# Optimization experiments

Hardware: AMD Instinct MI355X
Metric: run time of the kernel (lower is better)

Reference implementation:

```python
import jax, jax.numpy as jnp
import numpy as np

B, S, D = 4, 2048, 1024
H = 16
HD = D // H          # 64
HALF = HD // 2       # 32


def _rope(t, cos, sin):
    # t: [B, S, H, HD]; cos/sin: [S, HALF]
    tr = t.reshape(*t.shape[:-1], HALF, 2)
    t0, t1 = tr[..., 0], tr[..., 1]
    c = cos[None, :, None, :]
    s = sin[None, :, None, :]
    out = jnp.stack([t0 * c - t1 * s, t0 * s + t1 * c], axis=-1)
    return out.reshape(t.shape)


def setup_inputs() -> dict:
    key = jax.random.key(0)
    ks = jax.random.split(key, 7)
    x = jax.random.normal(ks[0], (B, S, D), dtype=jnp.float32)
    # rotary tables (theta=10000 convention)
    inv_freq = 1.0 / (10000.0 ** (np.arange(0, HD, 2, dtype=np.float32) / HD))
    angles = np.arange(S, dtype=np.float32)[:, None] * inv_freq[None, :]
    freqs_cos = jnp.asarray(np.cos(angles))
    freqs_sin = jnp.asarray(np.sin(angles))
    scale = 1.0 / np.sqrt(D)
    wq = jax.random.normal(ks[1], (D, D), dtype=jnp.float32) * scale
    wk = jax.random.normal(ks[2], (D, D), dtype=jnp.float32) * scale
    wv = jax.random.normal(ks[3], (D, D), dtype=jnp.float32) * scale
    wo = jax.random.normal(ks[4], (D, D), dtype=jnp.float32) * scale
    return {"x": x, "freqs_cos": freqs_cos, "freqs_sin": freqs_sin,
            "wq": wq, "wk": wk, "wv": wv, "wo": wo}


def reference(x, freqs_cos, freqs_sin, wq, wk, wv, wo):
    b, s, d = x.shape
    q = (x @ wq.T).reshape(b, s, H, HD)
    k = (x @ wk.T).reshape(b, s, H, HD)
    v = (x @ wv.T).reshape(b, s, H, HD)
    q = _rope(q, freqs_cos, freqs_sin)
    k = _rope(k, freqs_cos, freqs_sin)
    # [B, H, S, HD]
    q = q.transpose(0, 2, 1, 3)
    k = k.transpose(0, 2, 1, 3)
    v = v.transpose(0, 2, 1, 3)
    scores = jnp.einsum("bhqd,bhkd->bhqk", q, k) / jnp.sqrt(jnp.float32(HD))
    causal = jnp.tril(jnp.ones((s, s), dtype=bool))
    scores = jnp.where(causal[None, None, :, :], scores, jnp.finfo(scores.dtype).min)
    attn = jax.nn.softmax(scores, axis=-1)
    out = jnp.einsum("bhqk,bhkd->bhqd", attn, v)
    out = out.transpose(0, 2, 1, 3).reshape(b, s, d)
    return out @ wo.T
```

## Files before the change

### kernel.cpp

```cpp
#include <hip/hip_runtime.h>
#include <hip/hip_bf16.h>
#include <cstdint>
#include <cstddef>

#define BB 4
#define SS 2048
#define DD 1024
#define HH 16
#define HDD 64

typedef __bf16 bf16_t;
typedef __bf16 bf16x8 __attribute__((ext_vector_type(8)));
typedef float f32x4 __attribute__((ext_vector_type(4)));
typedef unsigned u32x2 __attribute__((ext_vector_type(2)));

__device__ __forceinline__ unsigned short f2bf(float f) {
    unsigned u = __float_as_uint(f);
    unsigned r = (u + 0x7FFFu + ((u >> 16) & 1u)) >> 16;
    return (unsigned short)r;
}
__device__ __forceinline__ bf16_t f2bf16(float f) {
    return __builtin_bit_cast(bf16_t, f2bf(f));
}
__device__ __forceinline__ bf16x8 cvt8(float4 a, float4 b) {
    bf16x8 r;
    r[0] = f2bf16(a.x); r[1] = f2bf16(a.y);
    r[2] = f2bf16(a.z); r[3] = f2bf16(a.w);
    r[4] = f2bf16(b.x); r[5] = f2bf16(b.y);
    r[6] = f2bf16(b.z); r[7] = f2bf16(b.w);
    return r;
}
__device__ __forceinline__ unsigned cvtpk_bf16(float lo, float hi) {
    unsigned r;
    asm("v_cvt_pk_bf16_f32 %0, %1, %2" : "=v"(r) : "v"(lo), "v"(hi));
    return r;
}
__device__ __forceinline__ float exp2_raw(float x) {
    float r;
    asm("v_exp_f32 %0, %1" : "=v"(r) : "v"(x));
    return r;
}

#define GLL16(gp, lp)                                                          \
    __builtin_amdgcn_global_load_lds(                                          \
        (const __attribute__((address_space(1))) void*)(gp),                   \
        (__attribute__((address_space(3))) void*)(lp), 16, 0, 0)

__global__ __launch_bounds__(256) void cvtall(
    const float* __restrict__ x,
    const float* __restrict__ w0, const float* __restrict__ w1,
    const float* __restrict__ w2, const float* __restrict__ w3,
    bf16_t* __restrict__ xb,
    bf16_t* __restrict__ o0, bf16_t* __restrict__ o1,
    bf16_t* __restrict__ o2, bf16_t* __restrict__ o3)
{
    const int bx = blockIdx.x;
    const float* in;
    bf16_t* out;
    size_t i;
    if (bx < 4096) {
        in = x; out = xb;
        i = (size_t)bx * 256 + threadIdx.x;
    } else {
        const int g = bx - 4096;
        const int s = g >> 9;
        in  = s == 0 ? w0 : s == 1 ? w1 : s == 2 ? w2 : w3;
        out = s == 0 ? o0 : s == 1 ? o1 : s == 2 ? o2 : o3;
        i = (size_t)(g & 511) * 256 + threadIdx.x;
    }
    const float4* p = (const float4*)in + i * 2;
    *(bf16x8*)(out + i * 8) = cvt8(p[0], p[1]);
}

__global__ __launch_bounds__(256, 2) void gemm_qkv(
    const bf16_t* __restrict__ A, const bf16_t* __restrict__ Wall,
    bf16_t* __restrict__ Qb, bf16_t* __restrict__ Kb,
    bf16_t* __restrict__ Vt,
    const float* __restrict__ fcos, const float* __restrict__ fsin,
    float qscale)
{
    constexpr int K = 1024;
    __shared__ alignas(16) bf16_t lA[128 * 64];
    __shared__ alignas(16) bf16_t lB[128 * 64];

    const int tid  = threadIdx.x;
    const int w    = tid >> 6;
    const int lane = tid & 63;
    const int quad = lane >> 4;
    const int l16  = lane & 15;
    const int wm   = w >> 1;
    const int wn   = w & 1;

    const int lid     = blockIdx.y * 24 + blockIdx.x;
    const int logical = (lid & 7) * 192 + (lid >> 3);
    const int m0      = (logical / 24) * 128;
    const int n0      = (logical % 24) * 128;
    const int sub     = n0 >> 10;

    f32x4 acc[4][4];
#pragma unroll
    for (int i = 0; i < 4; i++)
#pragma unroll
        for (int j = 0; j < 4; j++) acc[i][j] = (f32x4){0.f, 0.f, 0.f, 0.f};

    const int srow8 = lane >> 3;
    const int slot  = lane & 7;

    for (int k0 = 0; k0 < K; k0 += 64) {
#pragma unroll
        for (int i = 0; i < 4; ++i) {
            int rbase = w * 32 + i * 8;
            int row   = rbase + srow8;
            int sc    = (slot ^ (row & 7)) * 8;
            GLL16(A + (size_t)(m0 + row) * K + k0 + sc, &lA[rbase * 64]);
            GLL16(Wall + (size_t)(n0 + row) * K + k0 + sc, &lB[rbase * 64]);
        }
        __syncthreads();
#pragma unroll
        for (int kk = 0; kk < 2; ++kk) {
            bf16x8 af[4], bfr[4];
#pragma unroll
            for (int mt = 0; mt < 4; ++mt) {
                const int row = wm * 64 + mt * 16 + l16;
                af[mt] = *(const bf16x8*)
                    &lA[row * 64 + (((kk * 4 + quad) ^ (row & 7)) * 8)];
            }
#pragma unroll
            for (int nt = 0; nt < 4; ++nt) {
                const int row = wn * 64 + nt * 16 + l16;
                bfr[nt] = *(const bf16x8*)
                    &lB[row * 64 + (((kk * 4 + quad) ^ (row & 7)) * 8)];
            }
#pragma unroll
            for (int mt = 0; mt < 4; ++mt)
#pragma unroll
                for (int nt = 0; nt < 4; ++nt)
                    acc[mt][nt] = __builtin_amdgcn_mfma_f32_16x16x32_bf16(
                        af[mt], bfr[nt], acc[mt][nt], 0, 0, 0);
        }
        __syncthreads();
    }

    if (sub < 2) {
        unsigned short* Cu = (unsigned short*)(sub == 0 ? Qb : Kb);
        const float scale = sub == 0 ? qscale : 1.0f;
#pragma unroll
        for (int mt = 0; mt < 4; ++mt) {
#pragma unroll
            for (int nt = 0; nt < 4; ++nt) {
                int col  = (n0 & 1023) + wn * 64 + nt * 16 + l16;
                int h    = col >> 6;
                int d    = col & 63;
                int pidx = d >> 1;
                bool even = (col & 1) == 0;
#pragma unroll
                for (int r = 0; r < 4; ++r) {
                    int m = m0 + wm * 64 + mt * 16 + quad * 4 + r;
                    int b = m >> 11;
                    int s = m & 2047;
                    float v  = acc[mt][nt][r];
                    float p  = __shfl_xor(v, 1);
                    float c  = fcos[s * 32 + pidx];
                    float sn = fsin[s * 32 + pidx];
                    float o  = even ? (v * c - p * sn) : (p * sn + v * c);
                    Cu[(size_t)((b * HH + h) * SS + s) * HDD + d] =
                        f2bf(o * scale);
                }
            }
        }
    } else {
        unsigned short* Cu = (unsigned short*)Vt;
#pragma unroll
        for (int mt = 0; mt < 4; ++mt) {
#pragma unroll
            for (int nt = 0; nt < 4; ++nt) {
                int col = (n0 & 1023) + wn * 64 + nt * 16 + l16;
                int h = col >> 6, d = col & 63;
#pragma unroll
                for (int r = 0; r < 4; ++r) {
                    int m = m0 + wm * 64 + mt * 16 + quad * 4 + r;
                    int b = m >> 11, s = m & 2047;
                    Cu[(size_t)((b * HH + h) * HDD + d) * SS + s] =
                        f2bf(acc[mt][nt][r]);
                }
            }
        }
    }
}

__global__ __launch_bounds__(256, 2) void gemm_out(
    const bf16_t* __restrict__ A, const bf16_t* __restrict__ W,
    float* __restrict__ Cf)
{
    constexpr int K = 1024, N = 1024;
    __shared__ alignas(16) bf16_t lA[128 * 64];
    __shared__ alignas(16) bf16_t lB[128 * 64];

    const int tid  = threadIdx.x;
    const int w    = tid >> 6;
    const int lane = tid & 63;
    const int quad = lane >> 4;
    const int l16  = lane & 15;
    const int wm   = w >> 1;
    const int wn   = w & 1;

    const int lid     = blockIdx.y * 8 + blockIdx.x;
    const int logical = (lid & 7) * 64 + (lid >> 3);
    const int m0      = (logical >> 3) * 128;
    const int n0      = (logical & 7) * 128;

    f32x4 acc[4][4];
#pragma unroll
    for (int i = 0; i < 4; i++)
#pragma unroll
        for (int j = 0; j < 4; j++) acc[i][j] = (f32x4){0.f, 0.f, 0.f, 0.f};

    const int srow8 = lane >> 3;
    const int slot  = lane & 7;

    for (int k0 = 0; k0 < K; k0 += 64) {
#pragma unroll
        for (int i = 0; i < 4; ++i) {
            int rbase = w * 32 + i * 8;
            int row   = rbase + srow8;
            int sc    = (slot ^ (row & 7)) * 8;
            GLL16(A + (size_t)(m0 + row) * K + k0 + sc, &lA[rbase * 64]);
            GLL16(W + (size_t)(n0 + row) * K + k0 + sc, &lB[rbase * 64]);
        }
        __syncthreads();
#pragma unroll
        for (int kk = 0; kk < 2; ++kk) {
            bf16x8 af[4], bfr[4];
#pragma unroll
            for (int mt = 0; mt < 4; ++mt) {
                const int row = wm * 64 + mt * 16 + l16;
                af[mt] = *(const bf16x8*)
                    &lA[row * 64 + (((kk * 4 + quad) ^ (row & 7)) * 8)];
            }
#pragma unroll
            for (int nt = 0; nt < 4; ++nt) {
                const int row = wn * 64 + nt * 16 + l16;
                bfr[nt] = *(const bf16x8*)
                    &lB[row * 64 + (((kk * 4 + quad) ^ (row & 7)) * 8)];
            }
#pragma unroll
            for (int mt = 0; mt < 4; ++mt)
#pragma unroll
                for (int nt = 0; nt < 4; ++nt)
                    acc[mt][nt] = __builtin_amdgcn_mfma_f32_16x16x32_bf16(
                        af[mt], bfr[nt], acc[mt][nt], 0, 0, 0);
        }
        __syncthreads();
    }

#pragma unroll
    for (int mt = 0; mt < 4; ++mt) {
        int mrow = m0 + wm * 64 + mt * 16 + quad * 4;
#pragma unroll
        for (int nt = 0; nt < 4; ++nt) {
            int col = n0 + wn * 64 + nt * 16 + l16;
#pragma unroll
            for (int r = 0; r < 4; ++r)
                Cf[(size_t)(mrow + r) * N + col] = acc[mt][nt][r];
        }
    }
}

__global__ __launch_bounds__(256, 2) void attn(
    const bf16_t* __restrict__ Q, const bf16_t* __restrict__ Kt,
    const bf16_t* __restrict__ Vt, bf16_t* __restrict__ O)
{
    __shared__ alignas(16) bf16_t lK[128 * 64];
    __shared__ alignas(16) bf16_t lV[2][64 * 64];

    const int tid  = threadIdx.x;
    const int w    = tid >> 6;
    const int lane = tid & 63;
    const int quad = lane >> 4;
    const int l16  = lane & 15;

    const int blk  = blockIdx.x;
    const int xcd  = blk & 7;
    const int rest = blk >> 3;
    const int g    = rest & 7;
    const int bh   = ((rest >> 3) << 3) | xcd;

    const int b = bh >> 4, h = bh & 15;
    unsigned short* Ou = (unsigned short*)O;
    const bf16_t* Qb = Q  + (size_t)bh * SS * HDD;
    const bf16_t* Kb = Kt + (size_t)bh * SS * HDD;
    const bf16_t* Vb = Vt + (size_t)bh * HDD * SS;

    const int row8 = lane >> 3;
    const int chk  = lane & 7;

    for (int phase = 0; phase < 2; ++phase) {
        const int Tp  = phase ? 15 - g : g;
        const int q0  = Tp * 128 + w * 32;
        const int nkb = Tp + 1;

        bf16x8 qf[2][2];
#pragma unroll
        for (int qs = 0; qs < 2; ++qs) {
            const bf16_t* qp =
                Qb + (size_t)(q0 + qs * 16 + l16) * HDD + quad * 8;
            qf[qs][0] = *(const bf16x8*)(qp);
            qf[qs][1] = *(const bf16x8*)(qp + 32);
        }

        f32x4 o[2][4];
        float ps[2];
#pragma unroll
        for (int qs = 0; qs < 2; ++qs) {
            ps[qs] = 0.f;
#pragma unroll
            for (int i = 0; i < 4; ++i) o[qs][i] = (f32x4){0.f, 0.f, 0.f, 0.f};
        }

        for (int t = 0; t < nkb; ++t) {
            const int kb2 = t * 128;

#pragma unroll
            for (int i = 0; i < 4; ++i) {
                int rbase = w * 32 + i * 8;
                int row   = rbase + row8;
                GLL16(Kb + (size_t)(kb2 + row) * HDD + ((chk ^ (row & 7)) * 8),
                      &lK[rbase * 64]);
            }
#pragma unroll
            for (int pp = 0; pp < 2; ++pp)
#pragma unroll
                for (int i = 0; i < 2; ++i) {
                    int rbase = w * 16 + i * 8;
                    int row   = rbase + row8;
                    GLL16(Vb + (size_t)row * SS + kb2 + pp * 64 +
                              ((chk ^ (row & 7)) * 8),
                          &lV[pp][rbase * 64]);
                }
            __syncthreads();

#pragma unroll
            for (int p = 0; p < 2; ++p) {
                const int kbp = kb2 + p * 64;
                if (kbp < q0 + 32) {
                    const bool diag = (kbp + 63 > q0);

                    bf16x8 kf[4][2];
#pragma unroll
                    for (int nt = 0; nt < 4; ++nt) {
                        const int row = p * 64 + nt * 16 + l16;
#pragma unroll
                        for (int hf = 0; hf < 2; ++hf)
                            kf[nt][hf] = *(const bf16x8*)
                                &lK[row * 64 +
                                    (((hf * 4 + quad) ^ (row & 7)) * 8)];
                    }

                    unsigned pk[4][2][2];
#pragma unroll
                    for (int nt = 0; nt < 4; ++nt) {
                        const int krow = kbp + nt * 16 + quad * 4;
#pragma unroll
                        for (int qs = 0; qs < 2; ++qs) {
                            f32x4 s = (f32x4){0.f, 0.f, 0.f, 0.f};
                            s = __builtin_amdgcn_mfma_f32_16x16x32_bf16(
                                kf[nt][0], qf[qs][0], s, 0, 0, 0);
                            s = __builtin_amdgcn_mfma_f32_16x16x32_bf16(
                                kf[nt][1], qf[qs][1], s, 0, 0, 0);
                            if (diag) {
                                const int qcol = q0 + qs * 16 + l16;
#pragma unroll
                                for (int r = 0; r < 4; ++r)
                                    if (krow + r > qcol) s[r] = -1e30f;
                            }
                            float ev[4];
#pragma unroll
                            for (int r = 0; r < 4; ++r) {
                                float e = exp2_raw(s[r]);
                                ps[qs] += e;
                                ev[r] = e;
                            }
                            pk[nt][qs][0] = cvtpk_bf16(ev[0], ev[1]);
                            pk[nt][qs][1] = cvtpk_bf16(ev[2], ev[3]);
                        }
                    }

#pragma unroll
                    for (int kk = 0; kk < 2; ++kk) {
                        bf16x8 vfk[4];
#pragma unroll
                        for (int nt = 0; nt < 4; ++nt) {
                            const int row = nt * 16 + l16;
                            vfk[nt] = *(const bf16x8*)
                                &lV[p][row * 64 +
                                       (((kk * 4 + quad) ^ (row & 7)) * 8)];
                        }
#pragma unroll
                        for (int qs = 0; qs < 2; ++qs) {
                            u32x2 sA = __builtin_amdgcn_permlane32_swap(
                                pk[2 * kk][qs][0], pk[2 * kk + 1][qs][0],
                                false, false);
                            u32x2 sB = __builtin_amdgcn_permlane32_swap(
                                pk[2 * kk][qs][1], pk[2 * kk + 1][qs][1],
                                false, false);
                            u32x2 tA = __builtin_amdgcn_permlane16_swap(
                                sA.x, sA.y, false, false);
                            u32x2 tB = __builtin_amdgcn_permlane16_swap(
                                sB.x, sB.y, false, false);
                            union { unsigned d[4]; bf16x8 v; } pf;
                            pf.d[0] = tA.x;
                            pf.d[1] = tB.x;
                            pf.d[2] = tA.y;
                            pf.d[3] = tB.y;
#pragma unroll
                            for (int nt = 0; nt < 4; ++nt)
                                o[qs][nt] =
                                    __builtin_amdgcn_mfma_f32_16x16x32_bf16(
                                        pf.v, vfk[nt], o[qs][nt], 0, 0, 0);
                        }
                    }
                }
            }
            __syncthreads();
        }

#pragma unroll
        for (int qs = 0; qs < 2; ++qs) {
            float tsum = ps[qs];
            tsum += __shfl_xor(tsum, 16);
            tsum += __shfl_xor(tsum, 32);
            float inv[4];
#pragma unroll
            for (int r = 0; r < 4; ++r)
                inv[r] = 1.0f / __shfl(tsum, quad * 4 + r);
#pragma unroll
            for (int nt = 0; nt < 4; ++nt) {
                int d = nt * 16 + l16;
#pragma unroll
                for (int r = 0; r < 4; ++r) {
                    int s = q0 + qs * 16 + quad * 4 + r;
                    Ou[(size_t)(b * SS + s) * DD + h * HDD + d] =
                        f2bf(o[qs][nt][r] * inv[r]);
                }
            }
        }
    }
}

extern "C" void kernel_launch(void* const* d_in, const int* in_sizes, int n_in,
                              void* d_out, int out_size, void* d_ws,
                              size_t ws_size, hipStream_t stream)
{
    const float* x    = (const float*)d_in[0];
    const float* fcos = (const float*)d_in[1];
    const float* fsin = (const float*)d_in[2];
    const float* wq   = (const float*)d_in[3];
    const float* wk   = (const float*)d_in[4];
    const float* wv   = (const float*)d_in[5];
    const float* wo   = (const float*)d_in[6];

    char* ws = (char*)d_ws;
    const size_t TSZ = (size_t)BB * SS * DD * sizeof(bf16_t);
    const size_t WSZ = (size_t)DD * DD * sizeof(bf16_t);
    bf16_t* Qb  = (bf16_t*)(ws);
    bf16_t* Kb  = (bf16_t*)(ws + TSZ);
    bf16_t* Ob  = (bf16_t*)(ws + 2 * TSZ);
    bf16_t* wb0 = (bf16_t*)(ws + 3 * TSZ);
    bf16_t* wb1 = (bf16_t*)(ws + 3 * TSZ + WSZ);
    bf16_t* wb2 = (bf16_t*)(ws + 3 * TSZ + 2 * WSZ);
    bf16_t* wb3 = (bf16_t*)(ws + 3 * TSZ + 3 * WSZ);
    bf16_t* xb  = (bf16_t*)d_out;
    bf16_t* Vt  = (bf16_t*)((char*)d_out + TSZ);

    dim3 bb(256);
    cvtall<<<dim3(6144), bb, 0, stream>>>(x, wq, wk, wv, wo,
                                          xb, wb0, wb1, wb2, wb3);

    const float sscale = 0.125f * 1.44269504088896f;
    gemm_qkv<<<dim3(24, 64), bb, 0, stream>>>(xb, wb0, Qb, Kb, Vt,
                                              fcos, fsin, sscale);
    attn<<<dim3(512), bb, 0, stream>>>(Qb, Kb, Vt, Ob);
    gemm_out<<<dim3(8, 64), bb, 0, stream>>>(Ob, wb3, (float*)d_out);
}
```

Baseline: 229.6 us.

## Merge QKV and output GEMMs into templated 256x128 tile kernel with 8 waves

Replaces the two separate 128x128 GEMM kernels with one templated kernel using 512 threads and a 256-row M tile, sharing the B tile across twice as many rows. This is meant to cut global and LDS traffic per MFMA and halve the block count. The epilogue is selected by a template MODE: RoPE/scatter for QKV, or a plain fp32 store for the output projection. Larger LDS use and the doubled block size may reduce occupancy, and fewer blocks may underfill the GPU.

```diff
diff --git a/kernel.cpp b/kernel.cpp
--- a/kernel.cpp
+++ b/kernel.cpp
@@ -72,15 +72,16 @@
     *(bf16x8*)(out + i * 8) = cvt8(p[0], p[1]);
 }
 
-__global__ __launch_bounds__(256, 2) void gemm_qkv(
-    const bf16_t* __restrict__ A, const bf16_t* __restrict__ Wall,
+template <int MODE, int NT>
+__global__ __launch_bounds__(512, 2) void gemm256(
+    const bf16_t* __restrict__ A, const bf16_t* __restrict__ W,
     bf16_t* __restrict__ Qb, bf16_t* __restrict__ Kb,
-    bf16_t* __restrict__ Vt,
+    bf16_t* __restrict__ Vt, float* __restrict__ Cf,
     const float* __restrict__ fcos, const float* __restrict__ fsin,
     float qscale)
 {
     constexpr int K = 1024;
-    __shared__ alignas(16) bf16_t lA[128 * 64];
+    __shared__ alignas(16) bf16_t lA[256 * 64];
     __shared__ alignas(16) bf16_t lB[128 * 64];
 
     const int tid  = threadIdx.x;
@@ -91,11 +92,11 @@
     const int wm   = w >> 1;
     const int wn   = w & 1;
 
-    const int lid     = blockIdx.y * 24 + blockIdx.x;
-    const int logical = (lid & 7) * 192 + (lid >> 3);
-    const int m0      = (logical / 24) * 128;
-    const int n0      = (logical % 24) * 128;
-    const int sub     = n0 >> 10;
+    const int lid     = blockIdx.y * NT + blockIdx.x;
+    constexpr int CHK = (NT * 32) >> 3;
+    const int logical = (lid & 7) * CHK + (lid >> 3);
+    const int m0      = (logical / NT) * 256;
+    const int n0      = (logical % NT) * 128;
 
     f32x4 acc[4][4];
 #pragma unroll
@@ -103,17 +104,23 @@
 #pragma unroll
         for (int j = 0; j < 4; j++) acc[i][j] = (f32x4){0.f, 0.f, 0.f, 0.f};
 
-    const int srow8 = lane >> 3;
-    const int slot  = lane & 7;
+    const int row8 = lane >> 3;
+    const int chk  = lane & 7;
 
     for (int k0 = 0; k0 < K; k0 += 64) {
 #pragma unroll
         for (int i = 0; i < 4; ++i) {
             int rbase = w * 32 + i * 8;
-            int row   = rbase + srow8;
-            int sc    = (slot ^ (row & 7)) * 8;
-            GLL16(A + (size_t)(m0 + row) * K + k0 + sc, &lA[rbase * 64]);
-            GLL16(Wall + (size_t)(n0 + row) * K + k0 + sc, &lB[rbase * 64]);
+            int row   = rbase + row8;
+            GLL16(A + (size_t)(m0 + row) * K + k0 + ((chk ^ (row & 7)) * 8),
+                  &lA[rbase * 64]);
+        }
+#pragma unroll
+        for (int i = 0; i < 2; ++i) {
+            int rbase = w * 16 + i * 8;
+            int row   = rbase + row8;
+            GLL16(W + (size_t)(n0 + row) * K + k0 + ((chk ^ (row & 7)) * 8),
+                  &lB[rbase * 64]);
         }
         __syncthreads();
 #pragma unroll
@@ -141,127 +148,64 @@
         __syncthreads();
     }
 
-    if (sub < 2) {
-        unsigned short* Cu = (unsigned short*)(sub == 0 ? Qb : Kb);
-        const float scale = sub == 0 ? qscale : 1.0f;
+    if (MODE == 0) {
+        const int sub = n0 >> 10;
+        if (sub < 2) {
+            unsigned short* Cu = (unsigned short*)(sub == 0 ? Qb : Kb);
+            const float scale = sub == 0 ? qscale : 1.0f;
+#pragma unroll
+            for (int mt = 0; mt < 4; ++mt) {
+#pragma unroll
+                for (int nt = 0; nt < 4; ++nt) {
+                    int col  = (n0 & 1023) + wn * 64 + nt * 16 + l16;
+                    int h    = col >> 6;
+                    int d    = col & 63;
+                    int pidx = d >> 1;
+                    bool even = (col & 1) == 0;
+#pragma unroll
+                    for (int r = 0; r < 4; ++r) {
+                        int m = m0 + wm * 64 + mt * 16 + quad * 4 + r;
+                        int b = m >> 11;
+                        int s = m & 2047;
+                        float v  = acc[mt][nt][r];
+                        float p  = __shfl_xor(v, 1);
+                        float c  = fcos[s * 32 + pidx];
+                        float sn = fsin[s * 32 + pidx];
+                        float o  = even ? (v * c - p * sn) : (p * sn + v * c);
+                        Cu[(size_t)((b * HH + h) * SS + s) * HDD + d] =
+                            f2bf(o * scale);
+                    }
+                }
+            }
+        } else {
+            unsigned short* Cu = (unsigned short*)Vt;
+#pragma unroll
+            for (int mt = 0; mt < 4; ++mt) {
+#pragma unroll
+                for (int nt = 0; nt < 4; ++nt) {
+                    int col = (n0 & 1023) + wn * 64 + nt * 16 + l16;
+                    int h = col >> 6, d = col & 63;
+#pragma unroll
+                    for (int r = 0; r < 4; ++r) {
+                        int m = m0 + wm * 64 + mt * 16 + quad * 4 + r;
+                        int b = m >> 11, s = m & 2047;
+                        Cu[(size_t)((b * HH + h) * HDD + d) * SS + s] =
+                            f2bf(acc[mt][nt][r]);
+                    }
+                }
+            }
+        }
+    } else {
 #pragma unroll
         for (int mt = 0; mt < 4; ++mt) {
+            int mrow = m0 + wm * 64 + mt * 16 + quad * 4;
 #pragma unroll
             for (int nt = 0; nt < 4; ++nt) {
-                int col  = (n0 & 1023) + wn * 64 + nt * 16 + l16;
-                int h    = col >> 6;
-                int d    = col & 63;
-                int pidx = d >> 1;
-                bool even = (col & 1) == 0;
-#pragma unroll
-                for (int r = 0; r < 4; ++r) {
-                    int m = m0 + wm * 64 + mt * 16 + quad * 4 + r;
-                    int b = m >> 11;
-                    int s = m & 2047;
-                    float v  = acc[mt][nt][r];
-                    float p  = __shfl_xor(v, 1);
-                    float c  = fcos[s * 32 + pidx];
-                    float sn = fsin[s * 32 + pidx];
-                    float o  = even ? (v * c - p * sn) : (p * sn + v * c);
-                    Cu[(size_t)((b * HH + h) * SS + s) * HDD + d] =
-                        f2bf(o * scale);
-                }
-            }
-        }
-    } else {
-        unsigned short* Cu = (unsigned short*)Vt;
-#pragma unroll
-        for (int mt = 0; mt < 4; ++mt) {
-#pragma unroll
-            for (int nt = 0; nt < 4; ++nt) {
-                int col = (n0 & 1023) + wn * 64 + nt * 16 + l16;
-                int h = col >> 6, d = col & 63;
-#pragma unroll
-                for (int r = 0; r < 4; ++r) {
-                    int m = m0 + wm * 64 + mt * 16 + quad * 4 + r;
-                    int b = m >> 11, s = m & 2047;
-                    Cu[(size_t)((b * HH + h) * HDD + d) * SS + s] =
-                        f2bf(acc[mt][nt][r]);
-                }
-            }
-        }
-    }
-}
-
-__global__ __launch_bounds__(256, 2) void gemm_out(
-    const bf16_t* __restrict__ A, const bf16_t* __restrict__ W,
-    float* __restrict__ Cf)
-{
-    constexpr int K = 1024, N = 1024;
-    __shared__ alignas(16) bf16_t lA[128 * 64];
-    __shared__ alignas(16) bf16_t lB[128 * 64];
-
-    const int tid  = threadIdx.x;
-    const int w    = tid >> 6;
-    const int lane = tid & 63;
-    const int quad = lane >> 4;
-    const int l16  = lane & 15;
-    const int wm   = w >> 1;
-    const int wn   = w & 1;
-
-    const int lid     = blockIdx.y * 8 + blockIdx.x;
-    const int logical = (lid & 7) * 64 + (lid >> 3);
-    const int m0      = (logical >> 3) * 128;
-    const int n0      = (logical & 7) * 128;
-
-    f32x4 acc[4][4];
-#pragma unroll
-    for (int i = 0; i < 4; i++)
-#pragma unroll
-        for (int j = 0; j < 4; j++) acc[i][j] = (f32x4){0.f, 0.f, 0.f, 0.f};
-
-    const int srow8 = lane >> 3;
-    const int slot  = lane & 7;
-
-    for (int k0 = 0; k0 < K; k0 += 64) {
-#pragma unroll
-        for (int i = 0; i < 4; ++i) {
-            int rbase = w * 32 + i * 8;
-            int row   = rbase + srow8;
-            int sc    = (slot ^ (row & 7)) * 8;
-            GLL16(A + (size_t)(m0 + row) * K + k0 + sc, &lA[rbase * 64]);
-            GLL16(W + (size_t)(n0 + row) * K + k0 + sc, &lB[rbase * 64]);
-        }
-        __syncthreads();
-#pragma unroll
-        for (int kk = 0; kk < 2; ++kk) {
-            bf16x8 af[4], bfr[4];
-#pragma unroll
-            for (int mt = 0; mt < 4; ++mt) {
-                const int row = wm * 64 + mt * 16 + l16;
-                af[mt] = *(const bf16x8*)
-                    &lA[row * 64 + (((kk * 4 + quad) ^ (row & 7)) * 8)];
-            }
-#pragma unroll
-            for (int nt = 0; nt < 4; ++nt) {
-                const int row = wn * 64 + nt * 16 + l16;
-                bfr[nt] = *(const bf16x8*)
-                    &lB[row * 64 + (((kk * 4 + quad) ^ (row & 7)) * 8)];
-            }
-#pragma unroll
-            for (int mt = 0; mt < 4; ++mt)
-#pragma unroll
-                for (int nt = 0; nt < 4; ++nt)
-                    acc[mt][nt] = __builtin_amdgcn_mfma_f32_16x16x32_bf16(
-                        af[mt], bfr[nt], acc[mt][nt], 0, 0, 0);
-        }
-        __syncthreads();
-    }
-
-#pragma unroll
-    for (int mt = 0; mt < 4; ++mt) {
-        int mrow = m0 + wm * 64 + mt * 16 + quad * 4;
-#pragma unroll
-        for (int nt = 0; nt < 4; ++nt) {
-            int col = n0 + wn * 64 + nt * 16 + l16;
-#pragma unroll
-            for (int r = 0; r < 4; ++r)
-                Cf[(size_t)(mrow + r) * N + col] = acc[mt][nt][r];
+                int col = n0 + wn * 64 + nt * 16 + l16;
+#pragma unroll
+                for (int r = 0; r < 4; ++r)
+                    Cf[(size_t)(mrow + r) * 1024 + col] = acc[mt][nt][r];
+            }
         }
     }
 }
@@ -472,13 +416,14 @@
     bf16_t* xb  = (bf16_t*)d_out;
     bf16_t* Vt  = (bf16_t*)((char*)d_out + TSZ);
 
-    dim3 bb(256);
-    cvtall<<<dim3(6144), bb, 0, stream>>>(x, wq, wk, wv, wo,
-                                          xb, wb0, wb1, wb2, wb3);
+    cvtall<<<dim3(6144), dim3(256), 0, stream>>>(x, wq, wk, wv, wo,
+                                                 xb, wb0, wb1, wb2, wb3);
 
     const float sscale = 0.125f * 1.44269504088896f;
-    gemm_qkv<<<dim3(24, 64), bb, 0, stream>>>(xb, wb0, Qb, Kb, Vt,
-                                              fcos, fsin, sscale);
-    attn<<<dim3(512), bb, 0, stream>>>(Qb, Kb, Vt, Ob);
-    gemm_out<<<dim3(8, 64), bb, 0, stream>>>(Ob, wb3, (float*)d_out);
-}
+    gemm256<0, 24><<<dim3(24, 32), dim3(512), 0, stream>>>(
+        xb, wb0, Qb, Kb, Vt, nullptr, fcos, fsin, sscale);
+    attn<<<dim3(512), dim3(256), 0, stream>>>(Qb, Kb, Vt, Ob);
+    gemm256<1, 8><<<dim3(8, 32), dim3(512), 0, stream>>>(
+        Ob, wb3, nullptr, nullptr, nullptr, (float*)d_out,
+        fcos, fsin, 1.0f);
+}
```

After: 256.6 us. 11.8% more time.

## Pipeline QKV GEMM with 4-stage LDS ring and async prefetch

Applied to the files above, without the earlier changes.

Replaces the single-buffered K=64 loop in the QKV projection GEMM with a 4-slot ring of K=32 tiles. Loads run two tiles ahead, and fine-grained vmcnt waits with one barrier per step replace the two __syncthreads per iteration. MFMA sections are wrapped in s_setprio to favour math issue. This aims to hide global-to-LDS latency behind MFMA work. LDS per block stays at 32KB, but there are twice as many loop iterations and the reuse-before-overwrite safety depends on the stage distance.

```diff
diff --git a/kernel.cpp b/kernel.cpp
--- a/kernel.cpp
+++ b/kernel.cpp
@@ -80,8 +80,9 @@
     float qscale)
 {
     constexpr int K = 1024;
-    __shared__ alignas(16) bf16_t lA[128 * 64];
-    __shared__ alignas(16) bf16_t lB[128 * 64];
+    constexpr int TILE = 128 * 32;
+    __shared__ alignas(16) bf16_t lA[4 * TILE];
+    __shared__ alignas(16) bf16_t lB[4 * TILE];
 
     const int tid  = threadIdx.x;
     const int w    = tid >> 6;
@@ -103,42 +104,59 @@
 #pragma unroll
         for (int j = 0; j < 4; j++) acc[i][j] = (f32x4){0.f, 0.f, 0.f, 0.f};
 
-    const int srow8 = lane >> 3;
-    const int slot  = lane & 7;
-
-    for (int k0 = 0; k0 < K; k0 += 64) {
-#pragma unroll
-        for (int i = 0; i < 4; ++i) {
-            int rbase = w * 32 + i * 8;
-            int row   = rbase + srow8;
-            int sc    = (slot ^ (row & 7)) * 8;
-            GLL16(A + (size_t)(m0 + row) * K + k0 + sc, &lA[rbase * 64]);
-            GLL16(Wall + (size_t)(n0 + row) * K + k0 + sc, &lB[rbase * 64]);
-        }
-        __syncthreads();
-#pragma unroll
-        for (int kk = 0; kk < 2; ++kk) {
-            bf16x8 af[4], bfr[4];
-#pragma unroll
-            for (int mt = 0; mt < 4; ++mt) {
-                const int row = wm * 64 + mt * 16 + l16;
-                af[mt] = *(const bf16x8*)
-                    &lA[row * 64 + (((kk * 4 + quad) ^ (row & 7)) * 8)];
-            }
-#pragma unroll
-            for (int nt = 0; nt < 4; ++nt) {
-                const int row = wn * 64 + nt * 16 + l16;
-                bfr[nt] = *(const bf16x8*)
-                    &lB[row * 64 + (((kk * 4 + quad) ^ (row & 7)) * 8)];
-            }
-#pragma unroll
-            for (int mt = 0; mt < 4; ++mt)
-#pragma unroll
-                for (int nt = 0; nt < 4; ++nt)
-                    acc[mt][nt] = __builtin_amdgcn_mfma_f32_16x16x32_bf16(
-                        af[mt], bfr[nt], acc[mt][nt], 0, 0, 0);
-        }
-        __syncthreads();
+    const int srow = lane >> 2;
+    const int sch  = lane & 3;
+
+    auto stageT = [&](int t) {
+        const int kb = t << 5;
+        bf16_t* lAb = &lA[(t & 3) * TILE];
+        bf16_t* lBb = &lB[(t & 3) * TILE];
+#pragma unroll
+        for (int i = 0; i < 2; ++i) {
+            const int rbase = w * 32 + i * 16;
+            const int row   = rbase + srow;
+            const int sc    = ((sch ^ ((row >> 1) & 3)) << 3);
+            GLL16(A    + (size_t)(m0 + row) * K + kb + sc, lAb + rbase * 32);
+            GLL16(Wall + (size_t)(n0 + row) * K + kb + sc, lBb + rbase * 32);
+        }
+    };
+
+    stageT(0);
+    stageT(1);
+
+    for (int t = 0; t < 32; ++t) {
+        if (t < 30) stageT(t + 2);
+        if (t < 30)
+            asm volatile("s_waitcnt vmcnt(8)" ::: "memory");
+        else if (t == 30)
+            asm volatile("s_waitcnt vmcnt(4)" ::: "memory");
+        else
+            asm volatile("s_waitcnt vmcnt(0)" ::: "memory");
+        __builtin_amdgcn_s_barrier();
+
+        const bf16_t* lAb = &lA[(t & 3) * TILE];
+        const bf16_t* lBb = &lB[(t & 3) * TILE];
+        bf16x8 af[4], bfr[4];
+#pragma unroll
+        for (int mt = 0; mt < 4; ++mt) {
+            const int row = wm * 64 + mt * 16 + l16;
+            af[mt] = *(const bf16x8*)
+                &lAb[row * 32 + ((quad ^ ((row >> 1) & 3)) << 3)];
+        }
+#pragma unroll
+        for (int nt = 0; nt < 4; ++nt) {
+            const int row = wn * 64 + nt * 16 + l16;
+            bfr[nt] = *(const bf16x8*)
+                &lBb[row * 32 + ((quad ^ ((row >> 1) & 3)) << 3)];
+        }
+        __builtin_amdgcn_s_setprio(1);
+#pragma unroll
+        for (int mt = 0; mt < 4; ++mt)
+#pragma unroll
+            for (int nt = 0; nt < 4; ++nt)
+                acc[mt][nt] = __builtin_amdgcn_mfma_f32_16x16x32_bf16(
+                    af[mt], bfr[nt], acc[mt][nt], 0, 0, 0);
+        __builtin_amdgcn_s_setprio(0);
     }
 
     if (sub < 2) {
@@ -472,13 +490,12 @@
     bf16_t* xb  = (bf16_t*)d_out;
     bf16_t* Vt  = (bf16_t*)((char*)d_out + TSZ);
 
-    dim3 bb(256);
-    cvtall<<<dim3(6144), bb, 0, stream>>>(x, wq, wk, wv, wo,
-                                          xb, wb0, wb1, wb2, wb3);
+    cvtall<<<dim3(6144), dim3(256), 0, stream>>>(x, wq, wk, wv, wo,
+                                                 xb, wb0, wb1, wb2, wb3);
 
     const float sscale = 0.125f * 1.44269504088896f;
-    gemm_qkv<<<dim3(24, 64), bb, 0, stream>>>(xb, wb0, Qb, Kb, Vt,
-                                              fcos, fsin, sscale);
-    attn<<<dim3(512), bb, 0, stream>>>(Qb, Kb, Vt, Ob);
-    gemm_out<<<dim3(8, 64), bb, 0, stream>>>(Ob, wb3, (float*)d_out);
-}
+    gemm_qkv<<<dim3(24, 64), dim3(256), 0, stream>>>(xb, wb0, Qb, Kb, Vt,
+                                                     fcos, fsin, sscale);
+    attn<<<dim3(512), dim3(256), 0, stream>>>(Qb, Kb, Vt, Ob);
+    gemm_out<<<dim3(8, 64), dim3(256), 0, stream>>>(Ob, wb3, (float*)d_out);
+}
```

Result: slower. 248.2 us (+8.1%).
